# Kernel optimization log

Hardware: AMD Instinct MI355X
Metric: run time of the kernel (lower is better)

Reference implementation:

```python
import jax, jax.numpy as jnp
import numpy as np

HEADS = 8
DIM_HEAD = 64
LA = 0.33
LD = 0.33
LG = 0.33


def setup_inputs() -> dict:
    key = jax.random.key(0)
    ks = jax.random.split(key, 6)
    B, N, D = 4, 1024, 512
    inner = HEADS * DIM_HEAD
    x = jax.random.normal(ks[0], (B, N, D), jnp.float32)
    mask = jax.random.uniform(ks[1], (B, N)) < 0.9
    # sparse 0/1 molecular adjacency
    adjacency_mat = (jax.random.uniform(ks[2], (B, N, N)) < 0.05).astype(jnp.float32)
    # positive pairwise distances
    distance_mat = jax.random.uniform(ks[3], (B, N, N), jnp.float32) * 5.0
    W_qkv = jax.random.normal(ks[4], (D, inner * 3), jnp.float32) * 0.02
    W_out = jax.random.normal(ks[5], (inner, D), jnp.float32) * 0.02
    b_out = jnp.zeros((D,), jnp.float32)
    return {"x": x, "mask": mask, "adjacency_mat": adjacency_mat,
            "distance_mat": distance_mat, "W_qkv": W_qkv, "W_out": W_out, "b_out": b_out}


def reference(x, mask, adjacency_mat, distance_mat, W_qkv, W_out, b_out):
    B, N, _ = x.shape
    scale = DIM_HEAD ** -0.5
    # 'b n (h qkv d)' split: reshape to (B, N, H, 3, Dh) then move heads forward
    qkv = (x @ W_qkv).reshape(B, N, HEADS, 3, DIM_HEAD)
    q, k, v = (jnp.transpose(qkv[..., i, :], (0, 2, 1, 3)) for i in range(3))
    dots = jnp.einsum('bhid,bhjd->bhij', q, k) * scale  # [B,H,N,N]
    big = jnp.finfo(dots.dtype).max
    m2 = mask[:, None, :, None] & mask[:, None, None, :]  # [B,1,N,N]
    dots = jnp.where(m2, dots, -big)
    attn = jax.nn.softmax(dots, axis=-1) * LA
    # adjacency masked to 0; distance masked to +max so exp(-t) -> 0
    adj = jnp.where(m2, adjacency_mat[:, None], 0.0)
    dist = jnp.where(m2, distance_mat[:, None], big)
    attn = attn + LG * adj + LD * jnp.exp(-dist)
    out = jnp.einsum('bhij,bhjd->bhid', attn, v)
    out = jnp.transpose(out, (0, 2, 1, 3)).reshape(B, N, HEADS * DIM_HEAD)
    return out @ W_out + b_out
```

## Files before the change

### kernel.cpp

```cpp
#include <hip/hip_runtime.h>
#include <hip/hip_bf16.h>

typedef __attribute__((ext_vector_type(8))) __bf16 bf16x8;
typedef __attribute__((ext_vector_type(8))) unsigned short ushort8;
typedef __attribute__((ext_vector_type(4))) float f32x4;

#define DEVFN static __device__ __forceinline__

constexpr int B_ = 4, N_ = 1024, H_ = 8, DH_ = 64, INNER_ = 512, QC_ = 1536;
constexpr int JS_ = 4;
constexpr float LA_ = 0.33f, LD_ = 0.33f, LG_ = 0.33f;
constexpr float SCALE2_ = 0.125f * 1.44269504088896f;
constexpr long OCP_STRIDE_ = (long)4096 * 512;
constexpr long LP_STRIDE_  = (long)4 * 8 * 1024;

DEVFN unsigned short f2b(float f){
  unsigned int u = __builtin_bit_cast(unsigned int, f);
  u += 0x7FFFu + ((u >> 16) & 1u);
  return (unsigned short)(u >> 16);
}
DEVFN float b2f(unsigned short s){
  unsigned int u = ((unsigned int)s) << 16;
  return __builtin_bit_cast(float, u);
}
DEVFN float fexp2(float x){
  float r; asm("v_exp_f32 %0, %1" : "=v"(r) : "v"(x)); return r;
}
DEVFN unsigned int pack2(float lo, float hi){
  union { unsigned int u; __bf16 h[2]; } z;
  z.h[0] = (__bf16)lo; z.h[1] = (__bf16)hi;
  return z.u;
}

DEVFN f32x4 mfma16(bf16x8 a, bf16x8 b, f32x4 c){
  return __builtin_amdgcn_mfma_f32_16x16x32_bf16(a, b, c, 0, 0, 0);
}

DEVFN bf16x8 ldsb8(const unsigned short* p){ return *(const bf16x8*)p; }

DEVFN void gload16(const unsigned short* g, unsigned short* l){
  __builtin_amdgcn_global_load_lds(
      (const __attribute__((address_space(1))) unsigned int*)g,
      (__attribute__((address_space(3))) unsigned int*)l, 16, 0, 0);
}

DEVFN void lds_barrier(){
  __builtin_amdgcn_sched_barrier(0);
  asm volatile("s_waitcnt lgkmcnt(0)\n\ts_barrier" ::: "memory");
  __builtin_amdgcn_sched_barrier(0);
}


DEVFN int detect_enc_w0(const unsigned char* m8, const int* m32, const float* mf,
                        int t, int* fsh){
  if (t < 64){
    unsigned char a = m8[t];
    int bb = m32[t];
    float c = mf[t];
    unsigned long long bad0 = __ballot(a > 1);
    unsigned long long one0 = __ballot(a == 1);
    unsigned long long bad1 = __ballot(bb != 0 && bb != 1);
    unsigned long long one1 = __ballot(bb == 1);
    unsigned long long bad2 = __ballot(c != 0.0f && c != 1.0f);
    unsigned long long one2 = __ballot(c == 1.0f);
    if (t == 0){
      int f = 0;
      if (bad0 == 0ull && __popcll(one0) > 42) f = 0;
      else if (bad1 == 0ull && __popcll(one1) > 42) f = 1;
      else if (bad2 == 0ull && __popcll(one2) > 42) f = 2;
      *fsh = f;
    }
  }
  __syncthreads();
  return *fsh;
}

__global__ void prep_k(const unsigned char* __restrict__ m8, const int* __restrict__ m32,
                       const float* __restrict__ mf, unsigned char* __restrict__ mv,
                       const float* __restrict__ x, unsigned short* __restrict__ xb,
                       const float* __restrict__ Wq, unsigned short* __restrict__ WqT,
                       const float* __restrict__ Wo, unsigned short* __restrict__ WoT)
{
  const int bid = blockIdx.x, t = threadIdx.x;
  if (bid < 16){
    __shared__ int fsh;
    int f = detect_enc_w0(m8, m32, mf, t, &fsh);
    int i = bid * 256 + t;
    unsigned char v;
    if (f == 0) v = (m8[i] != 0);
    else if (f == 1) v = (m32[i] != 0);
    else v = (mf[i] != 0.0f);
    mv[i] = v;
  } else if (bid < 2064){
    int i = (bid - 16) * 256 + t;
    float4 v = ((const float4*)x)[i];
    ushort4 o = { f2b(v.x), f2b(v.y), f2b(v.z), f2b(v.w) };
    ((ushort4*)xb)[i] = o;
  } else {
    const float* W; unsigned short* Wt; int K, Nn, bx, by;
    if (bid < 2832){ W = Wq; Wt = WqT; K = 512; Nn = 1536; int r = bid - 2064; bx = r % 48; by = r / 48; }
    else           { W = Wo; Wt = WoT; K = 512; Nn = 512;  int r = bid - 2832; bx = r % 16; by = r / 16; }
    __shared__ float tt[32][33];
    int nb = bx * 32, kb = by * 32;
    int tx = t & 31, ty = t >> 5;
    #pragma unroll
    for (int i = 0; i < 32; i += 8)
      tt[ty + i][tx] = W[(long)(kb + ty + i) * Nn + nb + tx];
    __syncthreads();
    #pragma unroll
    for (int i = 0; i < 32; i += 8)
      Wt[(long)(nb + ty + i) * K + kb + tx] = f2b(tt[tx][ty + i]);
  }
}

template<int MODE, int BM, int BN>
__global__ __launch_bounds__(256)
void gemm_bt_k(const unsigned short* __restrict__ A, const unsigned short* __restrict__ Bt,
               const float* __restrict__ Cin, void* __restrict__ Cout,
               const unsigned short* __restrict__ Op, const float* __restrict__ Lp,
               unsigned short* __restrict__ VtOut,
               int M, int Nn, int K, long azs, long bzs)
{
  constexpr int BK = 64;
  constexpr int WM = BM / 2, WN = BN / 2, MR = WM / 16, NR = WN / 16;
  __shared__ __attribute__((aligned(16))) unsigned short As[2][BM * BK];
  __shared__ __attribute__((aligned(16))) unsigned short Bs[2][BN * BK];
  const int bm = blockIdx.x * BM, bn = blockIdx.y * BN, z = blockIdx.z;
  const unsigned short* Ap = A + (long)z * azs;
  const unsigned short* Bp = Bt + (long)z * bzs;
  const int tid = threadIdx.x, w = tid >> 6, lane = tid & 63;
  const int l15 = lane & 15, lg = lane >> 4;
  const int wr = w >> 1, wc = w & 1;
  const int srow = lane >> 3;
  const int sk0 = ((lane & 7) ^ srow) * 8;
  const int rk0 = (lg ^ (l15 & 7)) * 8;
  const int rk1 = ((lg + 4) ^ (l15 & 7)) * 8;

  f32x4 acc[MR][NR] = {};

  for (int kk = 0;;){
    if (kk == 0){
      #pragma unroll
      for (int i = 0; i < BM / 32; i++){
        int r0 = i * 32 + w * 8;
        gload16(Ap + (long)(bm + r0 + srow) * K + sk0, &As[0][r0 * BK]);
      }
      #pragma unroll
      for (int i = 0; i < BN / 32; i++){
        int r0 = i * 32 + w * 8;
        gload16(Bp + (long)(bn + r0 + srow) * K + sk0, &Bs[0][r0 * BK]);
      }
      __syncthreads();
    }
    int cur = (kk / BK) & 1;
    if (kk + BK < K){
      #pragma unroll
      for (int i = 0; i < BM / 32; i++){
        int r0 = i * 32 + w * 8;
        gload16(Ap + (long)(bm + r0 + srow) * K + (kk + BK) + sk0, &As[cur ^ 1][r0 * BK]);
      }
      #pragma unroll
      for (int i = 0; i < BN / 32; i++){
        int r0 = i * 32 + w * 8;
        gload16(Bp + (long)(bn + r0 + srow) * K + (kk + BK) + sk0, &Bs[cur ^ 1][r0 * BK]);
      }
    }
    bf16x8 af[MR][2], bf[NR][2];
    #pragma unroll
    for (int m = 0; m < MR; m++){
      const unsigned short* p = &As[cur][(wr * WM + m * 16 + l15) * BK];
      af[m][0] = ldsb8(p + rk0); af[m][1] = ldsb8(p + rk1);
    }
    #pragma unroll
    for (int n = 0; n < NR; n++){
      const unsigned short* p = &Bs[cur][(wc * WN + n * 16 + l15) * BK];
      bf[n][0] = ldsb8(p + rk0); bf[n][1] = ldsb8(p + rk1);
    }
    #pragma unroll
    for (int m = 0; m < MR; m++)
      #pragma unroll
      for (int n = 0; n < NR; n++){
        acc[m][n] = mfma16(af[m][0], bf[n][0], acc[m][n]);
        acc[m][n] = mfma16(af[m][1], bf[n][1], acc[m][n]);
      }
    kk += BK;
    if (kk >= K) break;
    __syncthreads();
  }

  #pragma unroll
  for (int m = 0; m < MR; m++)
    #pragma unroll
    for (int n = 0; n < NR; n++){
      int row0 = bm + wr * WM + m * 16 + lg * 4;
      int col = bn + wc * WN + n * 16 + l15;
      if (MODE == 0){
        ushort4 o;
        unsigned short* op = (unsigned short*)&o;
        #pragma unroll
        for (int r = 0; r < 4; r++){
          op[r] = f2b(acc[m][n][r]);
          ((unsigned short*)Cout)[(long)(row0 + r) * Nn + col] = op[r];
        }
        int hm = col % 192;
        if (hm >= 128){
          int bb = row0 >> 10, j0 = row0 & (N_ - 1);
          int hd = (col / 192) * 64 + (hm - 128);
          *(ushort4*)(VtOut + ((long)bb * INNER_ + hd) * N_ + j0) = o;
        }
      } else if (MODE == 1){
        #pragma unroll
        for (int r = 0; r < 4; r++){
          int row = row0 + r;
          float v = acc[m][n][r];
          long obase = ((long)z * N_ + row) * INNER_ + col;
          long lbase = ((long)z * H_ + (col >> 6)) * N_ + row;
          float o = 0.f, l = 0.f;
          #pragma unroll
          for (int js = 0; js < JS_; js++){
            o += b2f(Op[js * OCP_STRIDE_ + obase]);
            l += Lp[js * LP_STRIDE_ + lbase];
          }
          v += LA_ * o / l;
          ((unsigned short*)Cout)[((long)z * N_ + row) * Nn + col] = f2b(v);
        }
      } else {
        #pragma unroll
        for (int r = 0; r < 4; r++)
          ((float*)Cout)[(long)(row0 + r) * Nn + col] = acc[m][n][r] + Cin[col];
      }
    }
}

__global__ __launch_bounds__(256)
void attn_madd_k(const unsigned short* __restrict__ QKV, const unsigned short* __restrict__ Vt,
                 const unsigned char* __restrict__ mv,
                 unsigned short* __restrict__ Ocp, float* __restrict__ Lp,
                 const unsigned char* __restrict__ m8, const int* __restrict__ m32,
                 const float* __restrict__ mf,
                 const float* __restrict__ adj, const float* __restrict__ dist,
                 unsigned short* __restrict__ Madd)
{
  __shared__ __attribute__((aligned(16))) unsigned short Ks[64][72];
  __shared__ __attribute__((aligned(16))) unsigned short Vs[64][72];
  __shared__ __attribute__((aligned(16))) unsigned short Ps[4][16][72];
  const int bid = blockIdx.x, tid = threadIdx.x;

  if (bid >= 2048){
    int f = detect_enc_w0(m8, m32, mf, tid, (int*)&Ps[0][0][0]);
    long i = (long)(bid - 2048) * 256 + tid;
    long e = i * 4;
    int b = (int)(e >> 20);
    int rem = (int)(e & (long)(N_ * N_ - 1));
    int row = rem >> 10, col0 = rem & (N_ - 1);
    float4 a = ((const float4*)adj)[i];
    float4 d = ((const float4*)dist)[i];
    bool mi, mc[4];
    if (f == 0){
      mi = m8[b * N_ + row] != 0;
      unsigned int pk = *(const unsigned int*)(m8 + b * N_ + col0);
      #pragma unroll
      for (int r = 0; r < 4; r++) mc[r] = ((pk >> (8 * r)) & 255u) != 0;
    } else if (f == 1){
      mi = m32[b * N_ + row] != 0;
      #pragma unroll
      for (int r = 0; r < 4; r++) mc[r] = m32[b * N_ + col0 + r] != 0;
    } else {
      mi = mf[b * N_ + row] != 0.0f;
      #pragma unroll
      for (int r = 0; r < 4; r++) mc[r] = mf[b * N_ + col0 + r] != 0.0f;
    }
    float va[4] = {a.x, a.y, a.z, a.w};
    float vd[4] = {d.x, d.y, d.z, d.w};
    ushort4 o;
    unsigned short* op = (unsigned short*)&o;
    #pragma unroll
    for (int r = 0; r < 4; r++){
      bool m2 = mi && mc[r];
      float v = m2 ? (LG_ * va[r] + LD_ * __expf(-vd[r])) : 0.0f;
      op[r] = f2b(v);
    }
    ((ushort4*)Madd)[i] = o;
    return;
  }

  const int qb = (bid & 15) * 64, h = (bid >> 4) & 7;
  const int zc = bid >> 7;
  const int b = zc & 3, js = zc >> 2;
  const int w = tid >> 6, lane = tid & 63;
  const int l15 = lane & 15, lg = lane >> 4;

  const long qrowA = (long)(b * N_ + qb + w * 16 + l15) * QC_ + h * 192;
  bf16x8 qf0 = *(const bf16x8*)(QKV + qrowA + lg * 8);
  bf16x8 qf1 = *(const bf16x8*)(QKV + qrowA + 32 + lg * 8);

  const bool rv1 = mv[b * N_ + qb + w * 16 + l15] != 0;

  float l_run = 0.f;
  f32x4 acc[4] = {};

  const unsigned short* Vbase = Vt + ((long)b * INNER_ + h * DH_) * N_;
  const int kr0 = tid >> 3, kr1 = kr0 + 32;
  const int ko = (tid & 7) * 8;

  ushort8 kreg0, kreg1, vreg0, vreg1;
  {
    const int jb0 = js * (N_ / JS_);
    kreg0 = *(const ushort8*)(QKV + (long)(b * N_ + jb0 + kr0) * QC_ + h * 192 + 64 + ko);
    kreg1 = *(const ushort8*)(QKV + (long)(b * N_ + jb0 + kr1) * QC_ + h * 192 + 64 + ko);
    vreg0 = *(const ushort8*)(Vbase + (long)kr0 * N_ + jb0 + ko);
    vreg1 = *(const ushort8*)(Vbase + (long)kr1 * N_ + jb0 + ko);
  }

  constexpr int NT = N_ / JS_ / 64;
  for (int jt = 0; jt < NT; jt++){
    const int jbase = js * (N_ / JS_) + jt * 64;
    lds_barrier();
    *(ushort8*)&Ks[kr0][ko] = kreg0;
    *(ushort8*)&Ks[kr1][ko] = kreg1;
    *(ushort8*)&Vs[kr0][ko] = vreg0;
    *(ushort8*)&Vs[kr1][ko] = vreg1;
    if (jt < NT - 1){
      const int jn = jbase + 64;
      kreg0 = *(const ushort8*)(QKV + (long)(b * N_ + jn + kr0) * QC_ + h * 192 + 64 + ko);
      kreg1 = *(const ushort8*)(QKV + (long)(b * N_ + jn + kr1) * QC_ + h * 192 + 64 + ko);
      vreg0 = *(const ushort8*)(Vbase + (long)kr0 * N_ + jn + ko);
      vreg1 = *(const ushort8*)(Vbase + (long)kr1 * N_ + jn + ko);
    }
    lds_barrier();

    f32x4 s[4];
    __builtin_amdgcn_s_setprio(1);
    #pragma unroll
    for (int ct = 0; ct < 4; ct++){
      bf16x8 k0 = ldsb8(&Ks[ct * 16 + l15][lg * 8]);
      bf16x8 k1 = ldsb8(&Ks[ct * 16 + l15][32 + lg * 8]);
      f32x4 zz = {};
      zz = mfma16(k0, qf0, zz);
      zz = mfma16(k1, qf1, zz);
      s[ct] = zz;
    }
    __builtin_amdgcn_s_setprio(0);

    unsigned int cvm[4];
    #pragma unroll
    for (int ct = 0; ct < 4; ct++)
      cvm[ct] = *(const unsigned int*)(mv + b * N_ + jbase + ct * 16 + lg * 4);

    float tsum = 0.f;
    unsigned int pw[4][2];
    #pragma unroll
    for (int ct = 0; ct < 4; ct++){
      float pv[4];
      #pragma unroll
      for (int r = 0; r < 4; r++){
        float x = s[ct][r] * SCALE2_;
        bool ck = ((cvm[ct] >> (8 * r)) & 255u) != 0;
        float sv = ck ? x : -3e38f;
        if (!rv1) sv = 0.0f;
        float p = fexp2(sv);
        tsum += p;
        pv[r] = p;
      }
      pw[ct][0] = pack2(pv[0], pv[1]);
      pw[ct][1] = pack2(pv[2], pv[3]);
    }
    tsum += __shfl_xor(tsum, 16);
    tsum += __shfl_xor(tsum, 32);
    l_run += tsum;

    #pragma unroll
    for (int ct = 0; ct < 4; ct++)
      #pragma unroll
      for (int p2 = 0; p2 < 2; p2++){
        int klo = ct * 16 + lg * 4 + 2 * p2;
        *(unsigned int*)&Ps[w][l15][klo] = pw[ct][p2];
      }

    asm volatile("s_waitcnt lgkmcnt(0)" ::: "memory");
    __builtin_amdgcn_sched_barrier(0);

    bf16x8 pf0 = ldsb8(&Ps[w][l15][lg * 8]);
    bf16x8 pf1 = ldsb8(&Ps[w][l15][32 + lg * 8]);
    __builtin_amdgcn_s_setprio(1);
    #pragma unroll
    for (int ct = 0; ct < 4; ct++){
      bf16x8 v0 = ldsb8(&Vs[ct * 16 + l15][lg * 8]);
      bf16x8 v1 = ldsb8(&Vs[ct * 16 + l15][32 + lg * 8]);
      acc[ct] = mfma16(pf0, v0, acc[ct]);
      acc[ct] = mfma16(pf1, v1, acc[ct]);
    }
    __builtin_amdgcn_s_setprio(0);
  }

  #pragma unroll
  for (int r = 0; r < 4; r++){
    long orow = (long)js * (OCP_STRIDE_ / INNER_) + b * N_ + qb + w * 16 + lg * 4 + r;
    #pragma unroll
    for (int ct = 0; ct < 4; ct++)
      Ocp[orow * INNER_ + h * DH_ + ct * 16 + l15] = f2b(acc[ct][r]);
  }
  if (lg == 0)
    Lp[(long)js * LP_STRIDE_ + ((long)b * H_ + h) * N_ + qb + w * 16 + l15] = l_run;
}

extern "C" void kernel_launch(void* const* d_in, const int* in_sizes, int n_in,
                              void* d_out, int out_size, void* d_ws, size_t ws_size,
                              hipStream_t stream)
{
  const float* x    = (const float*)d_in[0];
  const void*  msk  = d_in[1];
  const float* adj  = (const float*)d_in[2];
  const float* dst  = (const float*)d_in[3];
  const float* wqkv = (const float*)d_in[4];
  const float* wout = (const float*)d_in[5];
  const float* bout = (const float*)d_in[6];
  float* out = (float*)d_out;

  char* p = (char*)d_ws;
  unsigned short* QKV  = (unsigned short*)p;  p += (long)4096 * 1536 * 2;
  unsigned short* Xb   = (unsigned short*)p;  p += (long)4096 * 512 * 2;
  unsigned short* WqT  = (unsigned short*)p;  p += (long)1536 * 512 * 2;
  unsigned short* WoT  = (unsigned short*)p;  p += (long)512 * 512 * 2;
  unsigned short* Vt   = (unsigned short*)p;  p += (long)4 * 512 * 1024 * 2;
  unsigned short* Madd = (unsigned short*)p;  p += (long)4 * 1024 * 1024 * 2;
  unsigned short* Ocp  = (unsigned short*)p;  p += (long)JS_ * OCP_STRIDE_ * 2;
  float*          Lp   = (float*)p;           p += (long)JS_ * LP_STRIDE_ * 4;
  unsigned short* OcB  = (unsigned short*)p;  p += (long)4096 * 512 * 2;
  unsigned char*  mv   = (unsigned char*)p;   p += 4096;

  prep_k<<<3088, 256, 0, stream>>>((const unsigned char*)msk, (const int*)msk,
                                   (const float*)msk, mv, x, Xb, wqkv, WqT, wout, WoT);
  gemm_bt_k<0, 128, 64><<<dim3(32, 24, 1), 256, 0, stream>>>(
      Xb, WqT, nullptr, QKV, nullptr, nullptr, Vt, 4096, 1536, 512, 0, 0);
  attn_madd_k<<<6144, 256, 0, stream>>>(QKV, Vt, mv, Ocp, Lp,
                                        (const unsigned char*)msk, (const int*)msk,
                                        (const float*)msk, adj, dst, Madd);
  gemm_bt_k<1, 64, 64><<<dim3(16, 8, 4), 256, 0, stream>>>(
      Madd, Vt, nullptr, OcB, Ocp, Lp, nullptr, 1024, 512, 1024,
      (long)1024 * 1024, (long)512 * 1024);
  gemm_bt_k<2, 64, 64><<<dim3(64, 8, 1), 256, 0, stream>>>(
      OcB, WoT, bout, out, nullptr, nullptr, nullptr, 4096, 512, 512, 0, 0);
}
```

Baseline: 76.20 us.

## Halve key-split count and double-buffer K/V register prefetch in attention

Cuts the key-dimension split from 4 to 2, so each attention block walks twice as many key tiles and fewer partial outputs are written and later combined. The loop is unrolled by two with two register sets (A/B), so K/V loads run two tiles ahead to hide more global-load latency. In exchange, fewer attention blocks are launched, which lowers parallelism, and register pressure rises from the extra prefetch buffers.

```diff
diff --git a/kernel.cpp b/kernel.cpp
--- a/kernel.cpp
+++ b/kernel.cpp
@@ -8,7 +8,7 @@
 #define DEVFN static __device__ __forceinline__
 
 constexpr int B_ = 4, N_ = 1024, H_ = 8, DH_ = 64, INNER_ = 512, QC_ = 1536;
-constexpr int JS_ = 4;
+constexpr int JS_ = 2;
 constexpr float LA_ = 0.33f, LD_ = 0.33f, LG_ = 0.33f;
 constexpr float SCALE2_ = 0.125f * 1.44269504088896f;
 constexpr long OCP_STRIDE_ = (long)4096 * 512;
@@ -246,9 +246,9 @@
   __shared__ __attribute__((aligned(16))) unsigned short Ps[4][16][72];
   const int bid = blockIdx.x, tid = threadIdx.x;
 
-  if (bid >= 2048){
+  if (bid >= 1024){
     int f = detect_enc_w0(m8, m32, mf, tid, (int*)&Ps[0][0][0]);
-    long i = (long)(bid - 2048) * 256 + tid;
+    long i = (long)(bid - 1024) * 256 + tid;
     long e = i * 4;
     int b = (int)(e >> 20);
     int rem = (int)(e & (long)(N_ * N_ - 1));
@@ -300,98 +300,118 @@
   f32x4 acc[4] = {};
 
   const unsigned short* Vbase = Vt + ((long)b * INNER_ + h * DH_) * N_;
+  const unsigned short* Kbase = QKV + (long)b * N_ * QC_ + h * 192 + 64;
   const int kr0 = tid >> 3, kr1 = kr0 + 32;
   const int ko = (tid & 7) * 8;
-
-  ushort8 kreg0, kreg1, vreg0, vreg1;
+  const int jb0 = js * (N_ / JS_);
+  constexpr int NT = N_ / JS_ / 64;
+
+  ushort8 kA0, kA1, vA0, vA1, kB0, kB1, vB0, vB1;
   {
-    const int jb0 = js * (N_ / JS_);
-    kreg0 = *(const ushort8*)(QKV + (long)(b * N_ + jb0 + kr0) * QC_ + h * 192 + 64 + ko);
-    kreg1 = *(const ushort8*)(QKV + (long)(b * N_ + jb0 + kr1) * QC_ + h * 192 + 64 + ko);
-    vreg0 = *(const ushort8*)(Vbase + (long)kr0 * N_ + jb0 + ko);
-    vreg1 = *(const ushort8*)(Vbase + (long)kr1 * N_ + jb0 + ko);
-  }
-
-  constexpr int NT = N_ / JS_ / 64;
-  for (int jt = 0; jt < NT; jt++){
-    const int jbase = js * (N_ / JS_) + jt * 64;
+    kA0 = *(const ushort8*)(Kbase + (long)(jb0 + kr0) * QC_ + ko);
+    kA1 = *(const ushort8*)(Kbase + (long)(jb0 + kr1) * QC_ + ko);
+    vA0 = *(const ushort8*)(Vbase + (long)kr0 * N_ + jb0 + ko);
+    vA1 = *(const ushort8*)(Vbase + (long)kr1 * N_ + jb0 + ko);
+    const int j1 = jb0 + 64;
+    kB0 = *(const ushort8*)(Kbase + (long)(j1 + kr0) * QC_ + ko);
+    kB1 = *(const ushort8*)(Kbase + (long)(j1 + kr1) * QC_ + ko);
+    vB0 = *(const ushort8*)(Vbase + (long)kr0 * N_ + j1 + ko);
+    vB1 = *(const ushort8*)(Vbase + (long)kr1 * N_ + j1 + ko);
+  }
+
+#define ATTN_COMPUTE(JBASE)                                                   \
+  {                                                                           \
+    f32x4 s[4];                                                               \
+    __builtin_amdgcn_s_setprio(1);                                            \
+    _Pragma("unroll")                                                         \
+    for (int ct = 0; ct < 4; ct++){                                           \
+      bf16x8 k0 = ldsb8(&Ks[ct * 16 + l15][lg * 8]);                          \
+      bf16x8 k1 = ldsb8(&Ks[ct * 16 + l15][32 + lg * 8]);                     \
+      f32x4 zz = {};                                                          \
+      zz = mfma16(k0, qf0, zz);                                               \
+      zz = mfma16(k1, qf1, zz);                                               \
+      s[ct] = zz;                                                             \
+    }                                                                         \
+    __builtin_amdgcn_s_setprio(0);                                            \
+    unsigned int cvm[4];                                                      \
+    _Pragma("unroll")                                                         \
+    for (int ct = 0; ct < 4; ct++)                                            \
+      cvm[ct] = *(const unsigned int*)(mv + b * N_ + (JBASE) + ct * 16 + lg * 4); \
+    float tsum = 0.f;                                                         \
+    unsigned int pw[4][2];                                                    \
+    _Pragma("unroll")                                                         \
+    for (int ct = 0; ct < 4; ct++){                                           \
+      float pv[4];                                                            \
+      _Pragma("unroll")                                                       \
+      for (int r = 0; r < 4; r++){                                            \
+        float xx = s[ct][r] * SCALE2_;                                        \
+        bool ck = ((cvm[ct] >> (8 * r)) & 255u) != 0;                         \
+        float sv = ck ? xx : -3e38f;                                          \
+        if (!rv1) sv = 0.0f;                                                  \
+        float pp = fexp2(sv);                                                 \
+        tsum += pp;                                                           \
+        pv[r] = pp;                                                           \
+      }                                                                       \
+      pw[ct][0] = pack2(pv[0], pv[1]);                                        \
+      pw[ct][1] = pack2(pv[2], pv[3]);                                        \
+    }                                                                         \
+    tsum += __shfl_xor(tsum, 16);                                             \
+    tsum += __shfl_xor(tsum, 32);                                             \
+    l_run += tsum;                                                            \
+    _Pragma("unroll")                                                         \
+    for (int ct = 0; ct < 4; ct++)                                            \
+      _Pragma("unroll")                                                       \
+      for (int p2 = 0; p2 < 2; p2++){                                         \
+        int klo = ct * 16 + lg * 4 + 2 * p2;                                  \
+        *(unsigned int*)&Ps[w][l15][klo] = pw[ct][p2];                        \
+      }                                                                       \
+    asm volatile("s_waitcnt lgkmcnt(0)" ::: "memory");                        \
+    __builtin_amdgcn_sched_barrier(0);                                        \
+    bf16x8 pf0 = ldsb8(&Ps[w][l15][lg * 8]);                                  \
+    bf16x8 pf1 = ldsb8(&Ps[w][l15][32 + lg * 8]);                             \
+    __builtin_amdgcn_s_setprio(1);                                            \
+    _Pragma("unroll")                                                         \
+    for (int ct = 0; ct < 4; ct++){                                           \
+      bf16x8 v0 = ldsb8(&Vs[ct * 16 + l15][lg * 8]);                          \
+      bf16x8 v1 = ldsb8(&Vs[ct * 16 + l15][32 + lg * 8]);                     \
+      acc[ct] = mfma16(pf0, v0, acc[ct]);                                     \
+      acc[ct] = mfma16(pf1, v1, acc[ct]);                                     \
+    }                                                                         \
+    __builtin_amdgcn_s_setprio(0);                                            \
+  }
+
+  for (int jt = 0; jt < NT; jt += 2){
+    const int jbase = jb0 + jt * 64;
     lds_barrier();
-    *(ushort8*)&Ks[kr0][ko] = kreg0;
-    *(ushort8*)&Ks[kr1][ko] = kreg1;
-    *(ushort8*)&Vs[kr0][ko] = vreg0;
-    *(ushort8*)&Vs[kr1][ko] = vreg1;
-    if (jt < NT - 1){
-      const int jn = jbase + 64;
-      kreg0 = *(const ushort8*)(QKV + (long)(b * N_ + jn + kr0) * QC_ + h * 192 + 64 + ko);
-      kreg1 = *(const ushort8*)(QKV + (long)(b * N_ + jn + kr1) * QC_ + h * 192 + 64 + ko);
-      vreg0 = *(const ushort8*)(Vbase + (long)kr0 * N_ + jn + ko);
-      vreg1 = *(const ushort8*)(Vbase + (long)kr1 * N_ + jn + ko);
+    *(ushort8*)&Ks[kr0][ko] = kA0;
+    *(ushort8*)&Ks[kr1][ko] = kA1;
+    *(ushort8*)&Vs[kr0][ko] = vA0;
+    *(ushort8*)&Vs[kr1][ko] = vA1;
+    if (jt + 2 < NT){
+      const int jn = jbase + 128;
+      kA0 = *(const ushort8*)(Kbase + (long)(jn + kr0) * QC_ + ko);
+      kA1 = *(const ushort8*)(Kbase + (long)(jn + kr1) * QC_ + ko);
+      vA0 = *(const ushort8*)(Vbase + (long)kr0 * N_ + jn + ko);
+      vA1 = *(const ushort8*)(Vbase + (long)kr1 * N_ + jn + ko);
     }
     lds_barrier();
-
-    f32x4 s[4];
-    __builtin_amdgcn_s_setprio(1);
-    #pragma unroll
-    for (int ct = 0; ct < 4; ct++){
-      bf16x8 k0 = ldsb8(&Ks[ct * 16 + l15][lg * 8]);
-      bf16x8 k1 = ldsb8(&Ks[ct * 16 + l15][32 + lg * 8]);
-      f32x4 zz = {};
-      zz = mfma16(k0, qf0, zz);
-      zz = mfma16(k1, qf1, zz);
-      s[ct] = zz;
-    }
-    __builtin_amdgcn_s_setprio(0);
-
-    unsigned int cvm[4];
-    #pragma unroll
-    for (int ct = 0; ct < 4; ct++)
-      cvm[ct] = *(const unsigned int*)(mv + b * N_ + jbase + ct * 16 + lg * 4);
-
-    float tsum = 0.f;
-    unsigned int pw[4][2];
-    #pragma unroll
-    for (int ct = 0; ct < 4; ct++){
-      float pv[4];
-      #pragma unroll
-      for (int r = 0; r < 4; r++){
-        float x = s[ct][r] * SCALE2_;
-        bool ck = ((cvm[ct] >> (8 * r)) & 255u) != 0;
-        float sv = ck ? x : -3e38f;
-        if (!rv1) sv = 0.0f;
-        float p = fexp2(sv);
-        tsum += p;
-        pv[r] = p;
-      }
-      pw[ct][0] = pack2(pv[0], pv[1]);
-      pw[ct][1] = pack2(pv[2], pv[3]);
-    }
-    tsum += __shfl_xor(tsum, 16);
-    tsum += __shfl_xor(tsum, 32);
-    l_run += tsum;
-
-    #pragma unroll
-    for (int ct = 0; ct < 4; ct++)
-      #pragma unroll
-      for (int p2 = 0; p2 < 2; p2++){
-        int klo = ct * 16 + lg * 4 + 2 * p2;
-        *(unsigned int*)&Ps[w][l15][klo] = pw[ct][p2];
-      }
-
-    asm volatile("s_waitcnt lgkmcnt(0)" ::: "memory");
-    __builtin_amdgcn_sched_barrier(0);
-
-    bf16x8 pf0 = ldsb8(&Ps[w][l15][lg * 8]);
-    bf16x8 pf1 = ldsb8(&Ps[w][l15][32 + lg * 8]);
-    __builtin_amdgcn_s_setprio(1);
-    #pragma unroll
-    for (int ct = 0; ct < 4; ct++){
-      bf16x8 v0 = ldsb8(&Vs[ct * 16 + l15][lg * 8]);
-      bf16x8 v1 = ldsb8(&Vs[ct * 16 + l15][32 + lg * 8]);
-      acc[ct] = mfma16(pf0, v0, acc[ct]);
-      acc[ct] = mfma16(pf1, v1, acc[ct]);
-    }
-    __builtin_amdgcn_s_setprio(0);
-  }
+    ATTN_COMPUTE(jbase)
+    lds_barrier();
+    *(ushort8*)&Ks[kr0][ko] = kB0;
+    *(ushort8*)&Ks[kr1][ko] = kB1;
+    *(ushort8*)&Vs[kr0][ko] = vB0;
+    *(ushort8*)&Vs[kr1][ko] = vB1;
+    if (jt + 3 < NT){
+      const int jn = jbase + 192;
+      kB0 = *(const ushort8*)(Kbase + (long)(jn + kr0) * QC_ + ko);
+      kB1 = *(const ushort8*)(Kbase + (long)(jn + kr1) * QC_ + ko);
+      vB0 = *(const ushort8*)(Vbase + (long)kr0 * N_ + jn + ko);
+      vB1 = *(const ushort8*)(Vbase + (long)kr1 * N_ + jn + ko);
+    }
+    lds_barrier();
+    ATTN_COMPUTE(jbase + 64)
+  }
+#undef ATTN_COMPUTE
 
   #pragma unroll
   for (int r = 0; r < 4; r++){
@@ -433,7 +453,7 @@
                                    (const float*)msk, mv, x, Xb, wqkv, WqT, wout, WoT);
   gemm_bt_k<0, 128, 64><<<dim3(32, 24, 1), 256, 0, stream>>>(
       Xb, WqT, nullptr, QKV, nullptr, nullptr, Vt, 4096, 1536, 512, 0, 0);
-  attn_madd_k<<<6144, 256, 0, stream>>>(QKV, Vt, mv, Ocp, Lp,
+  attn_madd_k<<<5120, 256, 0, stream>>>(QKV, Vt, mv, Ocp, Lp,
                                         (const unsigned char*)msk, (const int*)msk,
                                         (const float*)msk, adj, dst, Madd);
   gemm_bt_k<1, 64, 64><<<dim3(16, 8, 4), 256, 0, stream>>>(
```

New measurement: 72.44 us. 4.9% less time.

## Process two query groups per wave to reuse K/V tiles and halve key splits

Applied to the files above, without the earlier changes.

Each attention block now covers 128 query rows: every wave handles two 16-row query groups against the same K/V tile held in LDS and registers. The key split factor drops from 4 to 2, so there are half as many partial outputs to write and reduce, and the grid shrinks to match. The goal is less K/V global and LDS traffic per query and less partial-result overhead. In exchange there are fewer attention blocks, each with a longer serial loop and more registers, with a launch bound of 3 blocks per CU.

```diff
diff --git a/kernel.cpp b/kernel.cpp
--- a/kernel.cpp
+++ b/kernel.cpp
@@ -8,7 +8,7 @@
 #define DEVFN static __device__ __forceinline__
 
 constexpr int B_ = 4, N_ = 1024, H_ = 8, DH_ = 64, INNER_ = 512, QC_ = 1536;
-constexpr int JS_ = 4;
+constexpr int JS_ = 2;
 constexpr float LA_ = 0.33f, LD_ = 0.33f, LG_ = 0.33f;
 constexpr float SCALE2_ = 0.125f * 1.44269504088896f;
 constexpr long OCP_STRIDE_ = (long)4096 * 512;
@@ -232,7 +232,7 @@
     }
 }
 
-__global__ __launch_bounds__(256)
+__global__ __launch_bounds__(256, 3)
 void attn_madd_k(const unsigned short* __restrict__ QKV, const unsigned short* __restrict__ Vt,
                  const unsigned char* __restrict__ mv,
                  unsigned short* __restrict__ Ocp, float* __restrict__ Lp,
@@ -246,9 +246,9 @@
   __shared__ __attribute__((aligned(16))) unsigned short Ps[4][16][72];
   const int bid = blockIdx.x, tid = threadIdx.x;
 
-  if (bid >= 2048){
+  if (bid >= 512){
     int f = detect_enc_w0(m8, m32, mf, tid, (int*)&Ps[0][0][0]);
-    long i = (long)(bid - 2048) * 256 + tid;
+    long i = (long)(bid - 512) * 256 + tid;
     long e = i * 4;
     int b = (int)(e >> 20);
     int rem = (int)(e & (long)(N_ * N_ - 1));
@@ -284,37 +284,42 @@
     return;
   }
 
-  const int qb = (bid & 15) * 64, h = (bid >> 4) & 7;
-  const int zc = bid >> 7;
+  const int qb = (bid & 7) * 128, h = (bid >> 3) & 7;
+  const int zc = bid >> 6;
   const int b = zc & 3, js = zc >> 2;
   const int w = tid >> 6, lane = tid & 63;
   const int l15 = lane & 15, lg = lane >> 4;
 
-  const long qrowA = (long)(b * N_ + qb + w * 16 + l15) * QC_ + h * 192;
-  bf16x8 qf0 = *(const bf16x8*)(QKV + qrowA + lg * 8);
-  bf16x8 qf1 = *(const bf16x8*)(QKV + qrowA + 32 + lg * 8);
-
-  const bool rv1 = mv[b * N_ + qb + w * 16 + l15] != 0;
-
-  float l_run = 0.f;
-  f32x4 acc[4] = {};
+  bf16x8 qf[2][2];
+  bool rv[2];
+  #pragma unroll
+  for (int qg = 0; qg < 2; qg++){
+    const long qr = (long)(b * N_ + qb + w * 32 + qg * 16 + l15) * QC_ + h * 192;
+    qf[qg][0] = *(const bf16x8*)(QKV + qr + lg * 8);
+    qf[qg][1] = *(const bf16x8*)(QKV + qr + 32 + lg * 8);
+    rv[qg] = mv[b * N_ + qb + w * 32 + qg * 16 + l15] != 0;
+  }
+
+  float l_run[2] = {0.f, 0.f};
+  f32x4 acc[2][4] = {};
 
   const unsigned short* Vbase = Vt + ((long)b * INNER_ + h * DH_) * N_;
+  const unsigned short* Kbase = QKV + (long)b * N_ * QC_ + h * 192 + 64;
   const int kr0 = tid >> 3, kr1 = kr0 + 32;
   const int ko = (tid & 7) * 8;
+  const int jb0 = js * (N_ / JS_);
+  constexpr int NT = N_ / JS_ / 64;
 
   ushort8 kreg0, kreg1, vreg0, vreg1;
   {
-    const int jb0 = js * (N_ / JS_);
-    kreg0 = *(const ushort8*)(QKV + (long)(b * N_ + jb0 + kr0) * QC_ + h * 192 + 64 + ko);
-    kreg1 = *(const ushort8*)(QKV + (long)(b * N_ + jb0 + kr1) * QC_ + h * 192 + 64 + ko);
+    kreg0 = *(const ushort8*)(Kbase + (long)(jb0 + kr0) * QC_ + ko);
+    kreg1 = *(const ushort8*)(Kbase + (long)(jb0 + kr1) * QC_ + ko);
     vreg0 = *(const ushort8*)(Vbase + (long)kr0 * N_ + jb0 + ko);
     vreg1 = *(const ushort8*)(Vbase + (long)kr1 * N_ + jb0 + ko);
   }
 
-  constexpr int NT = N_ / JS_ / 64;
   for (int jt = 0; jt < NT; jt++){
-    const int jbase = js * (N_ / JS_) + jt * 64;
+    const int jbase = jb0 + jt * 64;
     lds_barrier();
     *(ushort8*)&Ks[kr0][ko] = kreg0;
     *(ushort8*)&Ks[kr1][ko] = kreg1;
@@ -322,86 +327,97 @@
     *(ushort8*)&Vs[kr1][ko] = vreg1;
     if (jt < NT - 1){
       const int jn = jbase + 64;
-      kreg0 = *(const ushort8*)(QKV + (long)(b * N_ + jn + kr0) * QC_ + h * 192 + 64 + ko);
-      kreg1 = *(const ushort8*)(QKV + (long)(b * N_ + jn + kr1) * QC_ + h * 192 + 64 + ko);
+      kreg0 = *(const ushort8*)(Kbase + (long)(jn + kr0) * QC_ + ko);
+      kreg1 = *(const ushort8*)(Kbase + (long)(jn + kr1) * QC_ + ko);
       vreg0 = *(const ushort8*)(Vbase + (long)kr0 * N_ + jn + ko);
       vreg1 = *(const ushort8*)(Vbase + (long)kr1 * N_ + jn + ko);
     }
     lds_barrier();
 
-    f32x4 s[4];
-    __builtin_amdgcn_s_setprio(1);
+    bf16x8 kf[4][2];
     #pragma unroll
     for (int ct = 0; ct < 4; ct++){
-      bf16x8 k0 = ldsb8(&Ks[ct * 16 + l15][lg * 8]);
-      bf16x8 k1 = ldsb8(&Ks[ct * 16 + l15][32 + lg * 8]);
-      f32x4 zz = {};
-      zz = mfma16(k0, qf0, zz);
-      zz = mfma16(k1, qf1, zz);
-      s[ct] = zz;
-    }
-    __builtin_amdgcn_s_setprio(0);
-
+      kf[ct][0] = ldsb8(&Ks[ct * 16 + l15][lg * 8]);
+      kf[ct][1] = ldsb8(&Ks[ct * 16 + l15][32 + lg * 8]);
+    }
     unsigned int cvm[4];
     #pragma unroll
     for (int ct = 0; ct < 4; ct++)
       cvm[ct] = *(const unsigned int*)(mv + b * N_ + jbase + ct * 16 + lg * 4);
 
-    float tsum = 0.f;
-    unsigned int pw[4][2];
-    #pragma unroll
-    for (int ct = 0; ct < 4; ct++){
-      float pv[4];
-      #pragma unroll
-      for (int r = 0; r < 4; r++){
-        float x = s[ct][r] * SCALE2_;
-        bool ck = ((cvm[ct] >> (8 * r)) & 255u) != 0;
-        float sv = ck ? x : -3e38f;
-        if (!rv1) sv = 0.0f;
-        float p = fexp2(sv);
-        tsum += p;
-        pv[r] = p;
-      }
-      pw[ct][0] = pack2(pv[0], pv[1]);
-      pw[ct][1] = pack2(pv[2], pv[3]);
-    }
-    tsum += __shfl_xor(tsum, 16);
-    tsum += __shfl_xor(tsum, 32);
-    l_run += tsum;
-
-    #pragma unroll
-    for (int ct = 0; ct < 4; ct++)
-      #pragma unroll
-      for (int p2 = 0; p2 < 2; p2++){
-        int klo = ct * 16 + lg * 4 + 2 * p2;
-        *(unsigned int*)&Ps[w][l15][klo] = pw[ct][p2];
-      }
-
-    asm volatile("s_waitcnt lgkmcnt(0)" ::: "memory");
-    __builtin_amdgcn_sched_barrier(0);
-
-    bf16x8 pf0 = ldsb8(&Ps[w][l15][lg * 8]);
-    bf16x8 pf1 = ldsb8(&Ps[w][l15][32 + lg * 8]);
-    __builtin_amdgcn_s_setprio(1);
-    #pragma unroll
-    for (int ct = 0; ct < 4; ct++){
-      bf16x8 v0 = ldsb8(&Vs[ct * 16 + l15][lg * 8]);
-      bf16x8 v1 = ldsb8(&Vs[ct * 16 + l15][32 + lg * 8]);
-      acc[ct] = mfma16(pf0, v0, acc[ct]);
-      acc[ct] = mfma16(pf1, v1, acc[ct]);
-    }
-    __builtin_amdgcn_s_setprio(0);
+    #pragma unroll
+    for (int qg = 0; qg < 2; qg++){
+      f32x4 s[4];
+      __builtin_amdgcn_s_setprio(1);
+      #pragma unroll
+      for (int ct = 0; ct < 4; ct++){
+        f32x4 zz = {};
+        zz = mfma16(kf[ct][0], qf[qg][0], zz);
+        zz = mfma16(kf[ct][1], qf[qg][1], zz);
+        s[ct] = zz;
+      }
+      __builtin_amdgcn_s_setprio(0);
+
+      float tsum = 0.f;
+      unsigned int pw[4][2];
+      #pragma unroll
+      for (int ct = 0; ct < 4; ct++){
+        float pv[4];
+        #pragma unroll
+        for (int r = 0; r < 4; r++){
+          float xx = s[ct][r] * SCALE2_;
+          bool ck = ((cvm[ct] >> (8 * r)) & 255u) != 0;
+          float sv = ck ? xx : -3e38f;
+          if (!rv[qg]) sv = 0.0f;
+          float pp = fexp2(sv);
+          tsum += pp;
+          pv[r] = pp;
+        }
+        pw[ct][0] = pack2(pv[0], pv[1]);
+        pw[ct][1] = pack2(pv[2], pv[3]);
+      }
+      tsum += __shfl_xor(tsum, 16);
+      tsum += __shfl_xor(tsum, 32);
+      l_run[qg] += tsum;
+
+      asm volatile("s_waitcnt lgkmcnt(0)" ::: "memory");
+      __builtin_amdgcn_sched_barrier(0);
+      #pragma unroll
+      for (int ct = 0; ct < 4; ct++)
+        #pragma unroll
+        for (int p2 = 0; p2 < 2; p2++){
+          int klo = ct * 16 + lg * 4 + 2 * p2;
+          *(unsigned int*)&Ps[w][l15][klo] = pw[ct][p2];
+        }
+      asm volatile("s_waitcnt lgkmcnt(0)" ::: "memory");
+      __builtin_amdgcn_sched_barrier(0);
+
+      bf16x8 pf0 = ldsb8(&Ps[w][l15][lg * 8]);
+      bf16x8 pf1 = ldsb8(&Ps[w][l15][32 + lg * 8]);
+      __builtin_amdgcn_s_setprio(1);
+      #pragma unroll
+      for (int ct = 0; ct < 4; ct++){
+        bf16x8 v0 = ldsb8(&Vs[ct * 16 + l15][lg * 8]);
+        bf16x8 v1 = ldsb8(&Vs[ct * 16 + l15][32 + lg * 8]);
+        acc[qg][ct] = mfma16(pf0, v0, acc[qg][ct]);
+        acc[qg][ct] = mfma16(pf1, v1, acc[qg][ct]);
+      }
+      __builtin_amdgcn_s_setprio(0);
+    }
   }
 
   #pragma unroll
-  for (int r = 0; r < 4; r++){
-    long orow = (long)js * (OCP_STRIDE_ / INNER_) + b * N_ + qb + w * 16 + lg * 4 + r;
-    #pragma unroll
-    for (int ct = 0; ct < 4; ct++)
-      Ocp[orow * INNER_ + h * DH_ + ct * 16 + l15] = f2b(acc[ct][r]);
-  }
-  if (lg == 0)
-    Lp[(long)js * LP_STRIDE_ + ((long)b * H_ + h) * N_ + qb + w * 16 + l15] = l_run;
+  for (int qg = 0; qg < 2; qg++){
+    #pragma unroll
+    for (int r = 0; r < 4; r++){
+      long orow = (long)js * (OCP_STRIDE_ / INNER_) + b * N_ + qb + w * 32 + qg * 16 + lg * 4 + r;
+      #pragma unroll
+      for (int ct = 0; ct < 4; ct++)
+        Ocp[orow * INNER_ + h * DH_ + ct * 16 + l15] = f2b(acc[qg][ct][r]);
+    }
+    if (lg == 0)
+      Lp[(long)js * LP_STRIDE_ + ((long)b * H_ + h) * N_ + qb + w * 32 + qg * 16 + l15] = l_run[qg];
+  }
 }
 
 extern "C" void kernel_launch(void* const* d_in, const int* in_sizes, int n_in,
@@ -433,7 +449,7 @@
                                    (const float*)msk, mv, x, Xb, wqkv, WqT, wout, WoT);
   gemm_bt_k<0, 128, 64><<<dim3(32, 24, 1), 256, 0, stream>>>(
       Xb, WqT, nullptr, QKV, nullptr, nullptr, Vt, 4096, 1536, 512, 0, 0);
-  attn_madd_k<<<6144, 256, 0, stream>>>(QKV, Vt, mv, Ocp, Lp,
+  attn_madd_k<<<4608, 256, 0, stream>>>(QKV, Vt, mv, Ocp, Lp,
                                         (const unsigned char*)msk, (const int*)msk,
                                         (const float*)msk, adj, dst, Madd);
   gemm_bt_k<1, 64, 64><<<dim3(16, 8, 4), 256, 0, stream>>>(
```

Result: faster. 70.57 us (median of 2 runs) (-7.4%).
